# Kernel optimization log

Measured on AMD Instinct MI355X. Metric: run time of the kernel, lower is better.

## Reference

```python
import jax, jax.numpy as jnp
import numpy as np

EPS = 1e-5
J = 17


def build_adj(num_joints=J):
    edges = [(0, 1), (1, 2), (1, 3), (3, 4), (4, 5), (1, 6), (6, 7), (7, 8),
             (0, 9), (9, 10), (10, 11), (0, 12), (12, 13), (13, 14)]
    if num_joints > 15:
        edges.extend([(11, 15), (14, 16)])
    adj = np.eye(num_joints, dtype=np.float32)
    for i, j in edges:
        if i < num_joints and j < num_joints:
            adj[i, j] = 1.0
            adj[j, i] = 1.0
    adj = adj / adj.sum(axis=1, keepdims=True)
    return jnp.asarray(adj)


def _bn(x, g, b, m, v):
    # inference-mode BatchNorm2d over channel axis 1 of (B,C,T,J)
    scale = (g / jnp.sqrt(v + EPS))[None, :, None, None]
    shift = (b - m * g / jnp.sqrt(v + EPS))[None, :, None, None]
    return x * scale + shift


def _conv1x1(x, w, b):
    # x: (B,C,T,J), w: (O,C) -> (B,O,T,J)
    return jnp.einsum('oc,bctj->botj', w, x) + b[None, :, None, None]


def _tconv(x, w, b):
    # temporal conv kernel (3,1), padding (1,0); x: (B,C,T,J), w: (O,C,3)
    y = jax.lax.conv_general_dilated(
        x, w[:, :, :, None], window_strides=(1, 1),
        padding=[(1, 1), (0, 0)],
        dimension_numbers=('NCHW', 'OIHW', 'NCHW'))
    return y + b[None, :, None, None]


def _block(x, adj, sw, sb, sg, sbb, sm, sv, tw, tb, tg, tbb, tm, tv,
           rw, rb, rg, rbb, rm, rv):
    residual = _bn(_conv1x1(x, rw, rb), rg, rbb, rm, rv)
    y = jnp.einsum('bctj,jk->bctk', x, adj)
    y = jax.nn.relu(_bn(_conv1x1(y, sw, sb), sg, sbb, sm, sv))
    y = _bn(_tconv(y, tw, tb), tg, tbb, tm, tv)
    return jax.nn.relu(y + residual)  # dropout is identity in eval mode


def setup_inputs() -> dict:
    key = jax.random.key(0)
    ks = iter(jax.random.split(key, 64))
    B, T = 16, 2048

    def randn(shape, s=0.1):
        return jax.random.normal(next(ks), shape, dtype=jnp.float32) * s

    def bn_params(c):
        g = 1.0 + randn((c,), 0.05)
        b = randn((c,), 0.05)
        m = randn((c,), 0.1)
        v = jax.random.uniform(next(ks), (c,), minval=0.5, maxval=1.5)
        return g, b, m, v

    inp = {
        'x': jax.random.normal(next(ks), (B, 3, T, J), dtype=jnp.float32),
        'adj': build_adj(J),
    }
    # block 0: 3 -> 64
    inp['b0_sw'] = randn((64, 3)); inp['b0_sb'] = randn((64,), 0.02)
    inp['b0_sg'], inp['b0_sbb'], inp['b0_sm'], inp['b0_sv'] = bn_params(64)
    inp['b0_tw'] = randn((64, 64, 3), 0.05); inp['b0_tb'] = randn((64,), 0.02)
    inp['b0_tg'], inp['b0_tbb'], inp['b0_tm'], inp['b0_tv'] = bn_params(64)
    inp['b0_rw'] = randn((64, 3)); inp['b0_rb'] = randn((64,), 0.02)
    inp['b0_rg'], inp['b0_rbb'], inp['b0_rm'], inp['b0_rv'] = bn_params(64)
    # block 1: 64 -> 128
    inp['b1_sw'] = randn((128, 64), 0.05); inp['b1_sb'] = randn((128,), 0.02)
    inp['b1_sg'], inp['b1_sbb'], inp['b1_sm'], inp['b1_sv'] = bn_params(128)
    inp['b1_tw'] = randn((128, 128, 3), 0.03); inp['b1_tb'] = randn((128,), 0.02)
    inp['b1_tg'], inp['b1_tbb'], inp['b1_tm'], inp['b1_tv'] = bn_params(128)
    inp['b1_rw'] = randn((128, 64), 0.05); inp['b1_rb'] = randn((128,), 0.02)
    inp['b1_rg'], inp['b1_rbb'], inp['b1_rm'], inp['b1_rv'] = bn_params(128)
    # projection 128 -> 128
    inp['proj_w'] = randn((128, 128), 0.05); inp['proj_b'] = randn((128,), 0.02)
    return inp


def reference(x, adj,
              b0_sw, b0_sb, b0_sg, b0_sbb, b0_sm, b0_sv,
              b0_tw, b0_tb, b0_tg, b0_tbb, b0_tm, b0_tv,
              b0_rw, b0_rb, b0_rg, b0_rbb, b0_rm, b0_rv,
              b1_sw, b1_sb, b1_sg, b1_sbb, b1_sm, b1_sv,
              b1_tw, b1_tb, b1_tg, b1_tbb, b1_tm, b1_tv,
              b1_rw, b1_rb, b1_rg, b1_rbb, b1_rm, b1_rv,
              proj_w, proj_b):
    y = _block(x, adj, b0_sw, b0_sb, b0_sg, b0_sbb, b0_sm, b0_sv,
               b0_tw, b0_tb, b0_tg, b0_tbb, b0_tm, b0_tv,
               b0_rw, b0_rb, b0_rg, b0_rbb, b0_rm, b0_rv)
    y = _block(y, adj, b1_sw, b1_sb, b1_sg, b1_sbb, b1_sm, b1_sv,
               b1_tw, b1_tb, b1_tg, b1_tbb, b1_tm, b1_tv,
               b1_rw, b1_rb, b1_rg, b1_rbb, b1_rm, b1_rv)
    y = y.mean(axis=-1)            # (B, C, T)
    y = y.transpose(0, 2, 1)       # (B, T, C)
    return jnp.einsum('btc,ec->bte', y, proj_w) + proj_b  # (B, T, embed)
```

## Files before the change

kernel.cpp:

```cpp
#include <hip/hip_runtime.h>
#include <hip/hip_bf16.h>
#include <stdint.h>

typedef __attribute__((ext_vector_type(8))) short bf16x8;
typedef __attribute__((ext_vector_type(4))) float f32x4;

#define EPSB 1e-5f

#define W0TE_B   0u
#define W1SB_B   24576u
#define W1E_B    40960u
#define W1R_B    139264u
#define PROJW_B  155648u
#define WS0F_B   188416u
#define WR0F_B   189440u
#define BS0F_B   190464u
#define CB0F_B   190720u
#define BS1F_B   190976u
#define CB1F_B   191488u
#define SPT_B    192000u
#define MEANS_B  193536u
#define MEANS_PERB 524288ull
#define Y0_PERB  4456448ull

__device__ __forceinline__ float bf2f(unsigned int u16v) {
    union { unsigned int i; float f; } v; v.i = u16v << 16; return v.f;
}
__device__ __forceinline__ unsigned short f2bf(float f) {
    unsigned int x = __float_as_uint(f);
    x = x + 0x7fffu + ((x >> 16) & 1u);
    return (unsigned short)(x >> 16);
}
__device__ __forceinline__ unsigned pk2(float a, float b) {
    union { __hip_bfloat162 h; unsigned u; } v;
    v.h = __float22bfloat162_rn(make_float2(a, b));
    return v.u;
}
__device__ __forceinline__ int div17(int p) { return (p * 241) >> 12; }

struct PrepArgs {
    const float *sw0,*sb0,*sg0,*sbb0,*sm0,*sv0;
    const float *tw0,*tb0,*tg0,*tbb0,*tm0,*tv0;
    const float *rw0,*rb0,*rg0,*rbb0,*rm0,*rv0;
    const float *sw1,*sb1,*sg1,*sbb1,*sm1,*sv1;
    const float *tw1,*tb1,*tg1,*tbb1,*tm1,*tv1;
    const float *rw1,*rb1,*rg1,*rbb1,*rm1,*rv1;
    const float *projw;
    const float *adj;
    unsigned char* ws;
};

__global__ void prep_kernel(PrepArgs a) {
    const int g = blockIdx.x * 256 + threadIdx.x;
    unsigned short* W0TE  = (unsigned short*)(a.ws + W0TE_B);
    unsigned short* W1SBp = (unsigned short*)(a.ws + W1SB_B);
    unsigned short* W1Ep  = (unsigned short*)(a.ws + W1E_B);
    unsigned short* W1Rp  = (unsigned short*)(a.ws + W1R_B);
    unsigned short* PROJW = (unsigned short*)(a.ws + PROJW_B);
    float* WS0F = (float*)(a.ws + WS0F_B);
    float* WR0F = (float*)(a.ws + WR0F_B);
    float* BS0F = (float*)(a.ws + BS0F_B);
    float* CB0F = (float*)(a.ws + CB0F_B);
    float* BS1F = (float*)(a.ws + BS1F_B);
    float* CB1F = (float*)(a.ws + CB1F_B);
    float2* SPT = (float2*)(a.ws + SPT_B);

    if (g < 64) {
        int o = g;
        float scs = a.sg0[o] / sqrtf(a.sv0[o] + EPSB);
        BS0F[o] = scs * (a.sb0[o] - a.sm0[o]) + a.sbb0[o];
        for (int c = 0; c < 4; c++) WS0F[o*4+c] = (c < 3) ? scs * a.sw0[o*3+c] : 0.f;
        float tct = a.tg0[o] / sqrtf(a.tv0[o] + EPSB);
        float rcr = a.rg0[o] / sqrtf(a.rv0[o] + EPSB);
        CB0F[o] = tct * (a.tb0[o] - a.tm0[o]) + a.tbb0[o]
                + rcr * (a.rb0[o] - a.rm0[o]) + a.rbb0[o];
        for (int c = 0; c < 4; c++) WR0F[o*4+c] = (c < 3) ? rcr * a.rw0[o*3+c] : 0.f;
    } else if (g < 192) {
        int o = g - 64;
        float scs = a.sg1[o] / sqrtf(a.sv1[o] + EPSB);
        BS1F[o] = scs * (a.sb1[o] - a.sm1[o]) + a.sbb1[o];
        float tct = a.tg1[o] / sqrtf(a.tv1[o] + EPSB);
        float rcr = a.rg1[o] / sqrtf(a.rv1[o] + EPSB);
        CB1F[o] = tct * (a.tb1[o] - a.tm1[o]) + a.tbb1[o]
                + rcr * (a.rb1[o] - a.rm1[o]) + a.rbb1[o];
    } else if (g < 12480) {
        int idx = g - 192;
        int o = idx / 192, k = idx % 192, tap = k >> 6, c = k & 63;
        float tct = a.tg0[o] / sqrtf(a.tv0[o] + EPSB);
        W0TE[o*192 + k] = f2bf(tct * a.tw0[(o*64 + c)*3 + tap]);
    } else if (g < 20672) {
        int idx = g - 12480;
        int o = idx >> 6, c = idx & 63;
        float scs = a.sg1[o] / sqrtf(a.sv1[o] + EPSB);
        W1SBp[o*64 + c] = f2bf(scs * a.sw1[o*64 + c]);
    } else if (g < 69824) {
        int idx = g - 20672;
        int h = idx / 24576, r = idx % 24576;
        int o = r / 192, k = r % 192, tap = k >> 6, c = (h << 6) + (k & 63);
        float tct = a.tg1[o] / sqrtf(a.tv1[o] + EPSB);
        W1Ep[(h*128 + o)*192 + k] = f2bf(tct * a.tw1[(o*128 + c)*3 + tap]);
    } else if (g < 78016) {
        int idx = g - 69824;
        int o = idx >> 6, c = idx & 63;
        float rcr = a.rg1[o] / sqrtf(a.rv1[o] + EPSB);
        W1Rp[o*64 + c] = f2bf(rcr * a.rw1[o*64 + c]);
    } else if (g < 94400) {
        int idx = g - 78016;
        PROJW[idx] = f2bf(a.projw[idx]);
    } else if (g < 94417) {
        int j = g - 94400;
        int cnt = 0;
        for (int k = 0; k < 17; k++) {
            float v = a.adj[k*17 + j];
            if (v != 0.0f && cnt < 8) {
                SPT[j*8 + cnt] = make_float2(v, __uint_as_float((unsigned)k));
                cnt++;
            }
        }
        for (; cnt < 8; cnt++) SPT[j*8 + cnt] = make_float2(0.f, __uint_as_float(0u));
    }
}

__launch_bounds__(256, 3)
__global__ void b0_kernel(const float* __restrict__ x,
                          const unsigned char* __restrict__ ws,
                          unsigned short* __restrict__ Y0,
                          unsigned short* __restrict__ YG, int b0base) {
    __shared__ float xt[510];
    __shared__ float xg[510];
    __shared__ float2 sptA[136];
    __shared__ float2 sptB[136];
    __shared__ float Ws0s[256], Wr0s[256], bs0s[64], cb0s[64];
    __shared__ __align__(16) unsigned short s0[170*72];
    __shared__ __align__(16) unsigned short yst[136*72];

    const int tid = threadIdx.x;
    const int b_loc = blockIdx.x >> 8;
    const int b = b0base + b_loc;
    const int t0 = (blockIdx.x & 255) << 3;
    const int Pb = (t0 - 1) * 17;

    const int w = tid >> 6, l = tid & 63, lr = l & 15, lg = l >> 4;
    const int n = w*16 + lr;

    const unsigned short* W0TE = (const unsigned short*)(ws + W0TE_B);
    bf16x8 bfr[6];
    #pragma unroll
    for (int ks = 0; ks < 6; ks++)
        bfr[ks] = *(const bf16x8*)&W0TE[n*192 + ks*32 + lg*8];

    if (tid < 136) {
        float2 raw = ((const float2*)(ws + SPT_B))[tid];
        sptA[tid] = make_float2(raw.x, __uint_as_float(__float_as_uint(raw.y) * 4u));
        sptB[tid] = make_float2(raw.x, __uint_as_float(__float_as_uint(raw.y) * 144u));
    }
    Ws0s[tid] = ((const float*)(ws + WS0F_B))[tid];
    Wr0s[tid] = ((const float*)(ws + WR0F_B))[tid];
    if (tid < 64) {
        bs0s[tid] = ((const float*)(ws + BS0F_B))[tid];
        cb0s[tid] = ((const float*)(ws + CB0F_B))[tid];
    }
    #pragma unroll
    for (int it = 0; it < 2; it++) {
        int idx = tid + it*256;
        if (idx < 510) {
            int c = idx / 170, r = idx - c*170;
            int P = Pb + r;
            float v = 0.f;
            if (P >= 0 && P < 34816) v = x[(size_t)(b*3 + c)*34816 + P];
            xt[idx] = v;
        }
    }
    __syncthreads();
    #pragma unroll
    for (int it = 0; it < 2; it++) {
        int idx = tid + it*256;
        if (idx < 510) {
            int c = idx / 170, r = idx - c*170;
            int j = r - 17*div17(r);
            const char* rowb = (const char*)&xt[c*170 + (r - j)];
            float acc = 0.f;
            #pragma unroll
            for (int i = 0; i < 8; i++) {
                float2 e = sptA[j*8 + i];
                acc += e.x * *(const float*)(rowb + __float_as_uint(e.y));
            }
            xg[idx] = acc;
        }
    }
    __syncthreads();
    #pragma unroll
    for (int it = 0; it < 11; it++) {
        int idx = tid + it*256;
        if (idx < 2720) {
            int r = idx >> 4, cg = idx & 15, o0 = cg*4;
            int P = Pb + r;
            uint2 pkv = make_uint2(0u, 0u);
            if (P >= 0 && P < 34816) {
                float a0 = xg[r], a1 = xg[170 + r], a2 = xg[340 + r];
                float v0 = fmaxf(bs0s[o0]   + Ws0s[(o0  )*4]*a0 + Ws0s[(o0  )*4+1]*a1 + Ws0s[(o0  )*4+2]*a2, 0.f);
                float v1 = fmaxf(bs0s[o0+1] + Ws0s[(o0+1)*4]*a0 + Ws0s[(o0+1)*4+1]*a1 + Ws0s[(o0+1)*4+2]*a2, 0.f);
                float v2 = fmaxf(bs0s[o0+2] + Ws0s[(o0+2)*4]*a0 + Ws0s[(o0+2)*4+1]*a1 + Ws0s[(o0+2)*4+2]*a2, 0.f);
                float v3 = fmaxf(bs0s[o0+3] + Ws0s[(o0+3)*4]*a0 + Ws0s[(o0+3)*4+1]*a1 + Ws0s[(o0+3)*4+2]*a2, 0.f);
                pkv.x = pk2(v0, v1); pkv.y = pk2(v2, v3);
            }
            *(uint2*)&s0[r*72 + o0] = pkv;
        }
    }
    __syncthreads();
    {
        const float wr0 = Wr0s[n*4], wr1 = Wr0s[n*4+1], wr2 = Wr0s[n*4+2];
        const float cbn = cb0s[n];
        for (int mb = 0; mb < 9; mb++) {
            const int ra = mb*16 + lr;
            f32x4 acc = {0.f, 0.f, 0.f, 0.f};
            #pragma unroll
            for (int ks = 0; ks < 6; ks++) {
                int row = ra + (ks >> 1)*17; if (row > 169) row = 169;
                const int c0 = ((ks & 1) << 5) + lg*8;
                acc = __builtin_amdgcn_mfma_f32_16x16x32_bf16(
                    *(const bf16x8*)&s0[row*72 + c0], bfr[ks], acc, 0, 0, 0);
            }
            const int mbase = mb*16 + lg*4;
            #pragma unroll
            for (int i = 0; i < 4; i++) {
                const int m = mbase + i;
                if (m < 136) {
                    float v = acc[i] + cbn + wr0*xt[m+17] + wr1*xt[170+m+17] + wr2*xt[340+m+17];
                    yst[m*72 + n] = f2bf(fmaxf(v, 0.f));
                }
            }
        }
    }
    __syncthreads();
    #pragma unroll
    for (int it = 0; it < 5; it++) {
        int idx = tid + it*256;
        if (idx < 1088) {
            int m = idx >> 3, seg = idx & 7;
            uint4 v = *(const uint4*)&yst[m*72 + seg*8];
            *(uint4*)&Y0[((size_t)b_loc*34816 + t0*17 + m)*64 + seg*8] = v;
        }
    }
    #pragma unroll
    for (int it = 0; it < 9; it++) {
        int idx = tid + it*256;
        if (idx < 2176) {
            int p = idx >> 4, cg = idx & 15;
            int j = p - 17*div17(p);
            const char* rowb = (const char*)yst + (p - j)*144 + cg*8;
            float a0=0.f, a1=0.f, a2=0.f, a3=0.f;
            #pragma unroll
            for (int i = 0; i < 8; i++) {
                float2 e = sptB[j*8 + i];
                uint2 u = *(const uint2*)(rowb + __float_as_uint(e.y));
                a0 += e.x * __uint_as_float(u.x << 16);
                a1 += e.x * __uint_as_float(u.x & 0xffff0000u);
                a2 += e.x * __uint_as_float(u.y << 16);
                a3 += e.x * __uint_as_float(u.y & 0xffff0000u);
            }
            uint2 o; o.x = pk2(a0, a1); o.y = pk2(a2, a3);
            *(uint2*)&YG[((size_t)b_loc*34816 + t0*17 + p)*64 + cg*4] = o;
        }
    }
}

__launch_bounds__(512, 2)
__global__ void b1_kernel(const unsigned char* __restrict__ ws,
                          const unsigned short* __restrict__ Y0,
                          const unsigned short* __restrict__ YG,
                          unsigned short* __restrict__ MEANS) {
    __shared__ __align__(16) unsigned short smem[36720];
    unsigned short* ybuf  = smem;
    unsigned short* ygbuf = smem + 12240;
    unsigned short* s0buf = smem + 24480;
    __shared__ float cb1s[128], bs1s[128];

    const int tid = threadIdx.x;
    const int b_loc = blockIdx.x >> 6;
    const int ck = blockIdx.x & 63;

    const unsigned short* W1SBp = (const unsigned short*)(ws + W1SB_B);
    const unsigned short* W1Ep  = (const unsigned short*)(ws + W1E_B);
    const unsigned short* W1Rp  = (const unsigned short*)(ws + W1R_B);

    const int w = tid >> 6, l = tid & 63, lr = l & 15, lg = l >> 4;
    const int n = w*16 + lr;
    const int sNt = w & 3, sMh = w >> 2;
    const int nloc_s = sNt*16 + lr;

    if (tid < 128) {
        cb1s[tid] = ((const float*)(ws + CB1F_B))[tid];
        bs1s[tid] = ((const float*)(ws + BS1F_B))[tid];
    }
    bf16x8 rb0 = *(const bf16x8*)&W1Rp[n*64 + lg*8];
    bf16x8 rb1 = *(const bf16x8*)&W1Rp[n*64 + 32 + lg*8];

    uint4 pf[5];
    auto PF = [&](int t0n) {
        const int Pb = t0n*17 - 17;
        #pragma unroll
        for (int s = 0; s < 5; s++) {
            int idx = tid + s*512;
            uint4 v = make_uint4(0u,0u,0u,0u);
            if (idx < 1360) {
                int p = idx >> 3, seg = idx & 7;
                int P = Pb + p;
                if (P >= 0 && P < 34816)
                    v = *(const uint4*)&YG[((size_t)b_loc*34816 + P)*64 + seg*8];
            } else if (idx < 2448) {
                int p = (idx - 1360) >> 3, seg = (idx - 1360) & 7;
                v = *(const uint4*)&Y0[((size_t)b_loc*34816 + t0n*17 + p)*64 + seg*8];
            }
            pf[s] = v;
        }
    };
    PF(ck << 5);

    for (int tt = 0; tt < 4; tt++) {
        const int t0 = (ck << 5) + (tt << 3);
        const int Pb = (t0 - 1) * 17;

        #pragma unroll
        for (int s = 0; s < 5; s++) {
            int idx = tid + s*512;
            if (idx < 1360) {
                int p = idx >> 3, seg = idx & 7;
                *(uint4*)&ygbuf[p*72 + seg*8] = pf[s];
            } else if (idx < 2448) {
                int p = (idx - 1360) >> 3, seg = (idx - 1360) & 7;
                *(uint4*)&ybuf[(17 + p)*72 + seg*8] = pf[s];
            }
        }
        __syncthreads();

        if (tt < 3) PF(t0 + 8);

        f32x4 tacc[9];
        #pragma unroll
        for (int mb = 0; mb < 9; mb++) {
            const int row = 17 + mb*16 + lr;
            f32x4 acc = {0.f, 0.f, 0.f, 0.f};
            acc = __builtin_amdgcn_mfma_f32_16x16x32_bf16(*(const bf16x8*)&ybuf[row*72 + lg*8],      rb0, acc, 0, 0, 0);
            acc = __builtin_amdgcn_mfma_f32_16x16x32_bf16(*(const bf16x8*)&ybuf[row*72 + 32 + lg*8], rb1, acc, 0, 0, 0);
            tacc[mb] = acc;
        }
        {
            bf16x8 sbA = *(const bf16x8*)&W1SBp[(nloc_s)*64 + lg*8];
            bf16x8 sbB = *(const bf16x8*)&W1SBp[(nloc_s)*64 + 32 + lg*8];
            const float bias = bs1s[nloc_s];
            const int mbE = sMh ? 11 : 6;
            for (int mb = sMh ? 6 : 0; mb < mbE; mb++) {
                int ra = mb*16 + lr; if (ra > 169) ra = 169;
                f32x4 sa = {0.f, 0.f, 0.f, 0.f};
                sa = __builtin_amdgcn_mfma_f32_16x16x32_bf16(*(const bf16x8*)&ygbuf[ra*72 + lg*8],      sbA, sa, 0, 0, 0);
                sa = __builtin_amdgcn_mfma_f32_16x16x32_bf16(*(const bf16x8*)&ygbuf[ra*72 + 32 + lg*8], sbB, sa, 0, 0, 0);
                const int mbase = mb*16 + lg*4;
                #pragma unroll
                for (int i = 0; i < 4; i++) {
                    int m = mbase + i;
                    if (m < 170) {
                        int P = Pb + m;
                        float v = (P >= 0 && P < 34816) ? fmaxf(sa[i] + bias, 0.f) : 0.f;
                        s0buf[m*72 + nloc_s] = f2bf(v);
                    }
                }
            }
        }
        __syncthreads();

        {
            bf16x8 bfh[6];
            #pragma unroll
            for (int ks = 0; ks < 6; ks++)
                bfh[ks] = *(const bf16x8*)&W1Ep[n*192 + ks*32 + lg*8];
            #pragma unroll
            for (int mb = 0; mb < 9; mb++) {
                const int ma = mb*16 + lr;
                f32x4 acc = tacc[mb];
                #pragma unroll
                for (int ks = 0; ks < 6; ks++) {
                    int row = ma + (ks >> 1)*17; if (row > 169) row = 169;
                    const int c0 = ((ks & 1) << 5) + lg*8;
                    acc = __builtin_amdgcn_mfma_f32_16x16x32_bf16(
                        *(const bf16x8*)&s0buf[row*72 + c0], bfh[ks], acc, 0, 0, 0);
                }
                tacc[mb] = acc;
            }
        }
        {
            bf16x8 sbA = *(const bf16x8*)&W1SBp[(64 + nloc_s)*64 + lg*8];
            bf16x8 sbB = *(const bf16x8*)&W1SBp[(64 + nloc_s)*64 + 32 + lg*8];
            const float bias = bs1s[64 + nloc_s];
            const int mbE = sMh ? 11 : 6;
            for (int mb = sMh ? 6 : 0; mb < mbE; mb++) {
                int ra = mb*16 + lr; if (ra > 169) ra = 169;
                f32x4 sa = {0.f, 0.f, 0.f, 0.f};
                sa = __builtin_amdgcn_mfma_f32_16x16x32_bf16(*(const bf16x8*)&ygbuf[ra*72 + lg*8],      sbA, sa, 0, 0, 0);
                sa = __builtin_amdgcn_mfma_f32_16x16x32_bf16(*(const bf16x8*)&ygbuf[ra*72 + 32 + lg*8], sbB, sa, 0, 0, 0);
                const int mbase = mb*16 + lg*4;
                #pragma unroll
                for (int i = 0; i < 4; i++) {
                    int m = mbase + i;
                    if (m < 170) {
                        int P = Pb + m;
                        float v = (P >= 0 && P < 34816) ? fmaxf(sa[i] + bias, 0.f) : 0.f;
                        ybuf[m*72 + nloc_s] = f2bf(v);
                    }
                }
            }
        }
        __syncthreads();

        {
            bf16x8 bfh[6];
            #pragma unroll
            for (int ks = 0; ks < 6; ks++)
                bfh[ks] = *(const bf16x8*)&W1Ep[(128 + n)*192 + ks*32 + lg*8];
            #pragma unroll
            for (int mb = 0; mb < 9; mb++) {
                const int ma = mb*16 + lr;
                f32x4 acc = tacc[mb];
                #pragma unroll
                for (int ks = 0; ks < 6; ks++) {
                    int row = ma + (ks >> 1)*17; if (row > 169) row = 169;
                    const int c0 = ((ks & 1) << 5) + lg*8;
                    acc = __builtin_amdgcn_mfma_f32_16x16x32_bf16(
                        *(const bf16x8*)&ybuf[row*72 + c0], bfh[ks], acc, 0, 0, 0);
                }
                tacc[mb] = acc;
            }
        }
        {
            const float cb = cb1s[n];
            #pragma unroll
            for (int t = 0; t < 8; t++) {
                float s = 0.f;
                #pragma unroll
                for (int mb = 0; mb < 9; mb++) {
                    #pragma unroll
                    for (int i = 0; i < 4; i++) {
                        const int mlo = mb*16 + i;
                        if (mlo + 12 >= t*17 && mlo <= t*17 + 16 && mlo < 136) {
                            int m = mlo + lg*4;
                            bool in = (m >= t*17) && (m <= t*17 + 16) && (m < 136);
                            float v = fmaxf(tacc[mb][i] + cb, 0.f);
                            s += in ? v : 0.f;
                        }
                    }
                }
                s += __shfl_xor(s, 16, 64);
                s += __shfl_xor(s, 32, 64);
                if ((t & 3) == lg)
                    MEANS[((size_t)(b_loc*2048 + t0 + t))*128 + n] = f2bf(s * (1.f/17.f));
            }
        }
        __syncthreads();
    }
}

__launch_bounds__(256, 3)
__global__ void proj_kernel(const unsigned short* __restrict__ MEANS,
                            const unsigned char* __restrict__ ws,
                            const float* __restrict__ projb,
                            float* __restrict__ outp, int bt_base) {
    __shared__ __align__(16) unsigned short As[128*136];
    __shared__ float pbs[128];

    const int tid = threadIdx.x;
    const int m0 = blockIdx.x * 128;
    const int w = tid >> 6, l = tid & 63, lr = l & 15, lg = l >> 4;
    const unsigned short* PROJW = (const unsigned short*)(ws + PROJW_B);

    if (tid < 128) pbs[tid] = projb[tid];
    #pragma unroll
    for (int it = 0; it < 8; it++) {
        int idx = tid + it*256;
        int m = idx >> 4, seg = idx & 15;
        *(uint4*)&As[m*136 + seg*8] = *(const uint4*)&MEANS[(size_t)(m0 + m)*128 + seg*8];
    }
    __syncthreads();

    f32x4 acc[8][2];
    #pragma unroll
    for (int et = 0; et < 8; et++) {
        const int e = et*16 + lr;
        bf16x8 bf[4];
        #pragma unroll
        for (int kf = 0; kf < 4; kf++)
            bf[kf] = *(const bf16x8*)&PROJW[e*128 + kf*32 + lg*8];
        #pragma unroll
        for (int m2 = 0; m2 < 2; m2++) {
            const int ra = (w*2 + m2)*16 + lr;
            f32x4 a = {0.f, 0.f, 0.f, 0.f};
            #pragma unroll
            for (int kf = 0; kf < 4; kf++)
                a = __builtin_amdgcn_mfma_f32_16x16x32_bf16(
                    *(const bf16x8*)&As[ra*136 + kf*32 + lg*8], bf[kf], a, 0, 0, 0);
            acc[et][m2] = a;
        }
    }
    #pragma unroll
    for (int et = 0; et < 8; et++) {
        const int e = et*16 + lr;
        const float pb = pbs[e];
        #pragma unroll
        for (int m2 = 0; m2 < 2; m2++) {
            const int mbase = (w*2 + m2)*16 + lg*4;
            #pragma unroll
            for (int i = 0; i < 4; i++) {
                const int m = mbase + i;
                outp[(size_t)(bt_base + m0 + m)*128 + e] = acc[et][m2][i] + pb;
            }
        }
    }
}

extern "C" void kernel_launch(void* const* d_in, const int* in_sizes, int n_in,
                              void* d_out, int out_size, void* d_ws, size_t ws_size,
                              hipStream_t stream) {
    const float* x     = (const float*)d_in[0];
    const float* adj   = (const float*)d_in[1];
    const float* projb = (const float*)d_in[39];
    unsigned char* ws  = (unsigned char*)d_ws;

    PrepArgs pa;
    pa.sw0 = (const float*)d_in[2];  pa.sb0  = (const float*)d_in[3];
    pa.sg0 = (const float*)d_in[4];  pa.sbb0 = (const float*)d_in[5];
    pa.sm0 = (const float*)d_in[6];  pa.sv0  = (const float*)d_in[7];
    pa.tw0 = (const float*)d_in[8];  pa.tb0  = (const float*)d_in[9];
    pa.tg0 = (const float*)d_in[10]; pa.tbb0 = (const float*)d_in[11];
    pa.tm0 = (const float*)d_in[12]; pa.tv0  = (const float*)d_in[13];
    pa.rw0 = (const float*)d_in[14]; pa.rb0  = (const float*)d_in[15];
    pa.rg0 = (const float*)d_in[16]; pa.rbb0 = (const float*)d_in[17];
    pa.rm0 = (const float*)d_in[18]; pa.rv0  = (const float*)d_in[19];
    pa.sw1 = (const float*)d_in[20]; pa.sb1  = (const float*)d_in[21];
    pa.sg1 = (const float*)d_in[22]; pa.sbb1 = (const float*)d_in[23];
    pa.sm1 = (const float*)d_in[24]; pa.sv1  = (const float*)d_in[25];
    pa.tw1 = (const float*)d_in[26]; pa.tb1  = (const float*)d_in[27];
    pa.tg1 = (const float*)d_in[28]; pa.tbb1 = (const float*)d_in[29];
    pa.tm1 = (const float*)d_in[30]; pa.tv1  = (const float*)d_in[31];
    pa.rw1 = (const float*)d_in[32]; pa.rb1  = (const float*)d_in[33];
    pa.rg1 = (const float*)d_in[34]; pa.rbb1 = (const float*)d_in[35];
    pa.rm1 = (const float*)d_in[36]; pa.rv1  = (const float*)d_in[37];
    pa.projw = (const float*)d_in[38];
    pa.adj = adj;
    pa.ws = ws;

    prep_kernel<<<dim3(369), dim3(256), 0, stream>>>(pa);

    const size_t perb = MEANS_PERB + 2ull * Y0_PERB;
    int chunk = 16;
    while (chunk > 1 && (size_t)MEANS_B + (size_t)chunk * perb > ws_size) chunk >>= 1;

    unsigned short* MEANSp = (unsigned short*)(ws + MEANS_B);
    unsigned short* Y0p    = (unsigned short*)(ws + MEANS_B + (size_t)chunk * MEANS_PERB);
    unsigned short* YGp    = (unsigned short*)((unsigned char*)Y0p + (size_t)chunk * Y0_PERB);

    for (int cb = 0; cb < 16; cb += chunk) {
        b0_kernel<<<dim3(chunk * 256), dim3(256), 0, stream>>>(x, ws, Y0p, YGp, cb);
        b1_kernel<<<dim3(chunk * 64), dim3(512), 0, stream>>>(ws, Y0p, YGp, MEANSp);
        proj_kernel<<<dim3(chunk * 16), dim3(256), 0, stream>>>(MEANSp, ws, projb, (float*)d_out, cb * 2048);
    }
}
```

Measured before the change: 370.5 us.

## Fuse projection GEMM into b1 kernel and specialize non-edge time tiles

The separate projection kernel is removed. Per-timestep joint means are staged in shared memory and multiplied by the projection weights inside b1_kernel every two time tiles, so the bf16 MEANS buffer no longer round-trips through global memory and one launch per chunk goes away. The spatial-conv epilogues get a fast path without boundary checks for interior tiles. MFMA loops are wrapped in s_setprio to raise wave priority. The fused projection adds MFMA work and projb global loads to the b1 loop, and fp32 output stores are now narrow per-lane writes from many blocks.

```diff
diff --git a/kernel.cpp b/kernel.cpp
--- a/kernel.cpp
+++ b/kernel.cpp
@@ -19,8 +19,7 @@
 #define BS1F_B   190976u
 #define CB1F_B   191488u
 #define SPT_B    192000u
-#define MEANS_B  193536u
-#define MEANS_PERB 524288ull
+#define SCRATCH_B 193536u
 #define Y0_PERB  4456448ull
 
 __device__ __forceinline__ float bf2f(unsigned int u16v) {
@@ -269,20 +268,25 @@
 __global__ void b1_kernel(const unsigned char* __restrict__ ws,
                           const unsigned short* __restrict__ Y0,
                           const unsigned short* __restrict__ YG,
-                          unsigned short* __restrict__ MEANS) {
+                          const float* __restrict__ projb,
+                          float* __restrict__ outp, int b0base) {
     __shared__ __align__(16) unsigned short smem[36720];
+    __shared__ __align__(16) unsigned short meansP[16*136];
+    __shared__ float cb1s[128], bs1s[128];
+
     unsigned short* ybuf  = smem;
     unsigned short* ygbuf = smem + 12240;
     unsigned short* s0buf = smem + 24480;
-    __shared__ float cb1s[128], bs1s[128];
 
     const int tid = threadIdx.x;
     const int b_loc = blockIdx.x >> 6;
     const int ck = blockIdx.x & 63;
+    const int gb = b0base + b_loc;
 
     const unsigned short* W1SBp = (const unsigned short*)(ws + W1SB_B);
     const unsigned short* W1Ep  = (const unsigned short*)(ws + W1E_B);
     const unsigned short* W1Rp  = (const unsigned short*)(ws + W1R_B);
+    const unsigned short* PROJW = (const unsigned short*)(ws + PROJW_B);
 
     const int w = tid >> 6, l = tid & 63, lr = l & 15, lg = l >> 4;
     const int n = w*16 + lr;
@@ -298,14 +302,14 @@
 
     uint4 pf[5];
     auto PF = [&](int t0n) {
-        const int Pb = t0n*17 - 17;
+        const int Pbn = t0n*17 - 17;
         #pragma unroll
         for (int s = 0; s < 5; s++) {
             int idx = tid + s*512;
             uint4 v = make_uint4(0u,0u,0u,0u);
             if (idx < 1360) {
                 int p = idx >> 3, seg = idx & 7;
-                int P = Pb + p;
+                int P = Pbn + p;
                 if (P >= 0 && P < 34816)
                     v = *(const uint4*)&YG[((size_t)b_loc*34816 + P)*64 + seg*8];
             } else if (idx < 2448) {
@@ -320,6 +324,7 @@
     for (int tt = 0; tt < 4; tt++) {
         const int t0 = (ck << 5) + (tt << 3);
         const int Pb = (t0 - 1) * 17;
+        const bool edge = (Pb < 0) || (Pb + 169 >= 34816);
 
         #pragma unroll
         for (int s = 0; s < 5; s++) {
@@ -349,20 +354,35 @@
             bf16x8 sbA = *(const bf16x8*)&W1SBp[(nloc_s)*64 + lg*8];
             bf16x8 sbB = *(const bf16x8*)&W1SBp[(nloc_s)*64 + 32 + lg*8];
             const float bias = bs1s[nloc_s];
-            const int mbE = sMh ? 11 : 6;
-            for (int mb = sMh ? 6 : 0; mb < mbE; mb++) {
-                int ra = mb*16 + lr; if (ra > 169) ra = 169;
-                f32x4 sa = {0.f, 0.f, 0.f, 0.f};
-                sa = __builtin_amdgcn_mfma_f32_16x16x32_bf16(*(const bf16x8*)&ygbuf[ra*72 + lg*8],      sbA, sa, 0, 0, 0);
-                sa = __builtin_amdgcn_mfma_f32_16x16x32_bf16(*(const bf16x8*)&ygbuf[ra*72 + 32 + lg*8], sbB, sa, 0, 0, 0);
-                const int mbase = mb*16 + lg*4;
-                #pragma unroll
-                for (int i = 0; i < 4; i++) {
-                    int m = mbase + i;
-                    if (m < 170) {
-                        int P = Pb + m;
-                        float v = (P >= 0 && P < 34816) ? fmaxf(sa[i] + bias, 0.f) : 0.f;
-                        s0buf[m*72 + nloc_s] = f2bf(v);
+            const int mbS = sMh ? 6 : 0, mbE = sMh ? 11 : 6;
+            if (!edge) {
+                for (int mb = mbS; mb < mbE; mb++) {
+                    int ra = mb*16 + lr; if (ra > 169) ra = 169;
+                    f32x4 sa = {0.f, 0.f, 0.f, 0.f};
+                    sa = __builtin_amdgcn_mfma_f32_16x16x32_bf16(*(const bf16x8*)&ygbuf[ra*72 + lg*8],      sbA, sa, 0, 0, 0);
+                    sa = __builtin_amdgcn_mfma_f32_16x16x32_bf16(*(const bf16x8*)&ygbuf[ra*72 + 32 + lg*8], sbB, sa, 0, 0, 0);
+                    const int mbase = mb*16 + lg*4;
+                    #pragma unroll
+                    for (int i = 0; i < 4; i++) {
+                        int m = mbase + i;
+                        if (m < 170) s0buf[m*72 + nloc_s] = f2bf(fmaxf(sa[i] + bias, 0.f));
+                    }
+                }
+            } else {
+                for (int mb = mbS; mb < mbE; mb++) {
+                    int ra = mb*16 + lr; if (ra > 169) ra = 169;
+                    f32x4 sa = {0.f, 0.f, 0.f, 0.f};
+                    sa = __builtin_amdgcn_mfma_f32_16x16x32_bf16(*(const bf16x8*)&ygbuf[ra*72 + lg*8],      sbA, sa, 0, 0, 0);
+                    sa = __builtin_amdgcn_mfma_f32_16x16x32_bf16(*(const bf16x8*)&ygbuf[ra*72 + 32 + lg*8], sbB, sa, 0, 0, 0);
+                    const int mbase = mb*16 + lg*4;
+                    #pragma unroll
+                    for (int i = 0; i < 4; i++) {
+                        int m = mbase + i;
+                        if (m < 170) {
+                            int P = Pb + m;
+                            float v = (P >= 0 && P < 34816) ? fmaxf(sa[i] + bias, 0.f) : 0.f;
+                            s0buf[m*72 + nloc_s] = f2bf(v);
+                        }
                     }
                 }
             }
@@ -374,6 +394,7 @@
             #pragma unroll
             for (int ks = 0; ks < 6; ks++)
                 bfh[ks] = *(const bf16x8*)&W1Ep[n*192 + ks*32 + lg*8];
+            __builtin_amdgcn_s_setprio(1);
             #pragma unroll
             for (int mb = 0; mb < 9; mb++) {
                 const int ma = mb*16 + lr;
@@ -387,25 +408,41 @@
                 }
                 tacc[mb] = acc;
             }
+            __builtin_amdgcn_s_setprio(0);
         }
         {
             bf16x8 sbA = *(const bf16x8*)&W1SBp[(64 + nloc_s)*64 + lg*8];
             bf16x8 sbB = *(const bf16x8*)&W1SBp[(64 + nloc_s)*64 + 32 + lg*8];
             const float bias = bs1s[64 + nloc_s];
-            const int mbE = sMh ? 11 : 6;
-            for (int mb = sMh ? 6 : 0; mb < mbE; mb++) {
-                int ra = mb*16 + lr; if (ra > 169) ra = 169;
-                f32x4 sa = {0.f, 0.f, 0.f, 0.f};
-                sa = __builtin_amdgcn_mfma_f32_16x16x32_bf16(*(const bf16x8*)&ygbuf[ra*72 + lg*8],      sbA, sa, 0, 0, 0);
-                sa = __builtin_amdgcn_mfma_f32_16x16x32_bf16(*(const bf16x8*)&ygbuf[ra*72 + 32 + lg*8], sbB, sa, 0, 0, 0);
-                const int mbase = mb*16 + lg*4;
-                #pragma unroll
-                for (int i = 0; i < 4; i++) {
-                    int m = mbase + i;
-                    if (m < 170) {
-                        int P = Pb + m;
-                        float v = (P >= 0 && P < 34816) ? fmaxf(sa[i] + bias, 0.f) : 0.f;
-                        ybuf[m*72 + nloc_s] = f2bf(v);
+            const int mbS = sMh ? 6 : 0, mbE = sMh ? 11 : 6;
+            if (!edge) {
+                for (int mb = mbS; mb < mbE; mb++) {
+                    int ra = mb*16 + lr; if (ra > 169) ra = 169;
+                    f32x4 sa = {0.f, 0.f, 0.f, 0.f};
+                    sa = __builtin_amdgcn_mfma_f32_16x16x32_bf16(*(const bf16x8*)&ygbuf[ra*72 + lg*8],      sbA, sa, 0, 0, 0);
+                    sa = __builtin_amdgcn_mfma_f32_16x16x32_bf16(*(const bf16x8*)&ygbuf[ra*72 + 32 + lg*8], sbB, sa, 0, 0, 0);
+                    const int mbase = mb*16 + lg*4;
+                    #pragma unroll
+                    for (int i = 0; i < 4; i++) {
+                        int m = mbase + i;
+                        if (m < 170) ybuf[m*72 + nloc_s] = f2bf(fmaxf(sa[i] + bias, 0.f));
+                    }
+                }
+            } else {
+                for (int mb = mbS; mb < mbE; mb++) {
+                    int ra = mb*16 + lr; if (ra > 169) ra = 169;
+                    f32x4 sa = {0.f, 0.f, 0.f, 0.f};
+                    sa = __builtin_amdgcn_mfma_f32_16x16x32_bf16(*(const bf16x8*)&ygbuf[ra*72 + lg*8],      sbA, sa, 0, 0, 0);
+                    sa = __builtin_amdgcn_mfma_f32_16x16x32_bf16(*(const bf16x8*)&ygbuf[ra*72 + 32 + lg*8], sbB, sa, 0, 0, 0);
+                    const int mbase = mb*16 + lg*4;
+                    #pragma unroll
+                    for (int i = 0; i < 4; i++) {
+                        int m = mbase + i;
+                        if (m < 170) {
+                            int P = Pb + m;
+                            float v = (P >= 0 && P < 34816) ? fmaxf(sa[i] + bias, 0.f) : 0.f;
+                            ybuf[m*72 + nloc_s] = f2bf(v);
+                        }
                     }
                 }
             }
@@ -417,6 +454,7 @@
             #pragma unroll
             for (int ks = 0; ks < 6; ks++)
                 bfh[ks] = *(const bf16x8*)&W1Ep[(128 + n)*192 + ks*32 + lg*8];
+            __builtin_amdgcn_s_setprio(1);
             #pragma unroll
             for (int mb = 0; mb < 9; mb++) {
                 const int ma = mb*16 + lr;
@@ -430,9 +468,11 @@
                 }
                 tacc[mb] = acc;
             }
+            __builtin_amdgcn_s_setprio(0);
         }
         {
             const float cb = cb1s[n];
+            float mv0 = 0.f, mv1 = 0.f;
             #pragma unroll
             for (int t = 0; t < 8; t++) {
                 float s = 0.f;
@@ -451,66 +491,33 @@
                 }
                 s += __shfl_xor(s, 16, 64);
                 s += __shfl_xor(s, 32, 64);
-                if ((t & 3) == lg)
-                    MEANS[((size_t)(b_loc*2048 + t0 + t))*128 + n] = f2bf(s * (1.f/17.f));
-            }
+                float mval = s * (1.f / 17.f);
+                if (t == lg)     mv0 = mval;
+                if (t == lg + 4) mv1 = mval;
+            }
+            const int mrow = (tt & 1) * 8;
+            meansP[(mrow + lg)*136 + n]     = f2bf(mv0);
+            meansP[(mrow + 4 + lg)*136 + n] = f2bf(mv1);
         }
         __syncthreads();
-    }
-}
-
-__launch_bounds__(256, 3)
-__global__ void proj_kernel(const unsigned short* __restrict__ MEANS,
-                            const unsigned char* __restrict__ ws,
-                            const float* __restrict__ projb,
-                            float* __restrict__ outp, int bt_base) {
-    __shared__ __align__(16) unsigned short As[128*136];
-    __shared__ float pbs[128];
-
-    const int tid = threadIdx.x;
-    const int m0 = blockIdx.x * 128;
-    const int w = tid >> 6, l = tid & 63, lr = l & 15, lg = l >> 4;
-    const unsigned short* PROJW = (const unsigned short*)(ws + PROJW_B);
-
-    if (tid < 128) pbs[tid] = projb[tid];
-    #pragma unroll
-    for (int it = 0; it < 8; it++) {
-        int idx = tid + it*256;
-        int m = idx >> 4, seg = idx & 15;
-        *(uint4*)&As[m*136 + seg*8] = *(const uint4*)&MEANS[(size_t)(m0 + m)*128 + seg*8];
-    }
-    __syncthreads();
-
-    f32x4 acc[8][2];
-    #pragma unroll
-    for (int et = 0; et < 8; et++) {
-        const int e = et*16 + lr;
-        bf16x8 bf[4];
-        #pragma unroll
-        for (int kf = 0; kf < 4; kf++)
-            bf[kf] = *(const bf16x8*)&PROJW[e*128 + kf*32 + lg*8];
-        #pragma unroll
-        for (int m2 = 0; m2 < 2; m2++) {
-            const int ra = (w*2 + m2)*16 + lr;
-            f32x4 a = {0.f, 0.f, 0.f, 0.f};
+
+        if (tt & 1) {
+            const int et = w;
+            bf16x8 pw[4];
             #pragma unroll
             for (int kf = 0; kf < 4; kf++)
-                a = __builtin_amdgcn_mfma_f32_16x16x32_bf16(
-                    *(const bf16x8*)&As[ra*136 + kf*32 + lg*8], bf[kf], a, 0, 0, 0);
-            acc[et][m2] = a;
-        }
-    }
-    #pragma unroll
-    for (int et = 0; et < 8; et++) {
-        const int e = et*16 + lr;
-        const float pb = pbs[e];
-        #pragma unroll
-        for (int m2 = 0; m2 < 2; m2++) {
-            const int mbase = (w*2 + m2)*16 + lg*4;
+                pw[kf] = *(const bf16x8*)&PROJW[(et*16 + lr)*128 + kf*32 + lg*8];
+            f32x4 pa = {0.f, 0.f, 0.f, 0.f};
+            #pragma unroll
+            for (int kf = 0; kf < 4; kf++)
+                pa = __builtin_amdgcn_mfma_f32_16x16x32_bf16(
+                    *(const bf16x8*)&meansP[lr*136 + kf*32 + lg*8], pw[kf], pa, 0, 0, 0);
+            const float pb = projb[et*16 + lr];
+            const int tbase = ck*32 + (tt - 1)*8;
             #pragma unroll
             for (int i = 0; i < 4; i++) {
-                const int m = mbase + i;
-                outp[(size_t)(bt_base + m0 + m)*128 + e] = acc[et][m2][i] + pb;
+                const int m = lg*4 + i;
+                outp[((size_t)gb*2048 + tbase + m)*128 + et*16 + lr] = pa[i] + pb;
             }
         }
     }
@@ -538,8 +545,9 @@
     pa.sg1 = (const float*)d_in[22]; pa.sbb1 = (const float*)d_in[23];
     pa.sm1 = (const float*)d_in[24]; pa.sv1  = (const float*)d_in[25];
     pa.tw1 = (const float*)d_in[26]; pa.tb1  = (const float*)d_in[27];
-    pa.tg1 = (const float*)d_in[28]; pa.tbb1 = (const float*)d_in[29];
-    pa.tm1 = (const float*)d_in[30]; pa.tv1  = (const float*)d_in[31];
+    pa.tm1 = (const float*)d_in[30]; pa.tbb1 = (const float*)d_in[29];
+    pa.tg1 = (const float*)d_in[28];
+    pa.tv1  = (const float*)d_in[31];
     pa.rw1 = (const float*)d_in[32]; pa.rb1  = (const float*)d_in[33];
     pa.rg1 = (const float*)d_in[34]; pa.rbb1 = (const float*)d_in[35];
     pa.rm1 = (const float*)d_in[36]; pa.rv1  = (const float*)d_in[37];
@@ -549,17 +557,15 @@
 
     prep_kernel<<<dim3(369), dim3(256), 0, stream>>>(pa);
 
-    const size_t perb = MEANS_PERB + 2ull * Y0_PERB;
+    const size_t perb = 2ull * Y0_PERB;
     int chunk = 16;
-    while (chunk > 1 && (size_t)MEANS_B + (size_t)chunk * perb > ws_size) chunk >>= 1;
-
-    unsigned short* MEANSp = (unsigned short*)(ws + MEANS_B);
-    unsigned short* Y0p    = (unsigned short*)(ws + MEANS_B + (size_t)chunk * MEANS_PERB);
-    unsigned short* YGp    = (unsigned short*)((unsigned char*)Y0p + (size_t)chunk * Y0_PERB);
+    while (chunk > 1 && (size_t)SCRATCH_B + (size_t)chunk * perb > ws_size) chunk >>= 1;
+
+    unsigned short* Y0p = (unsigned short*)(ws + SCRATCH_B);
+    unsigned short* YGp = (unsigned short*)((unsigned char*)Y0p + (size_t)chunk * Y0_PERB);
 
     for (int cb = 0; cb < 16; cb += chunk) {
         b0_kernel<<<dim3(chunk * 256), dim3(256), 0, stream>>>(x, ws, Y0p, YGp, cb);
-        b1_kernel<<<dim3(chunk * 64), dim3(512), 0, stream>>>(ws, Y0p, YGp, MEANSp);
-        proj_kernel<<<dim3(chunk * 16), dim3(256), 0, stream>>>(MEANSp, ws, projb, (float*)d_out, cb * 2048);
-    }
-}
+        b1_kernel<<<dim3(chunk * 64), dim3(512), 0, stream>>>(ws, Y0p, YGp, projb, (float*)d_out, cb);
+    }
+}
```

New measurement: 353.0 us. 1.05x faster.
